# Performance work log

Measured on AMD Instinct MI355X. Metric: run time of the kernel, lower is better.

## Reference

```python
import jax, jax.numpy as jnp
import numpy as np

BS, H, S, DK = 4, 16, 1024, 64  # bs, n_heads, seq_len(=q_len), head_dim


def setup_inputs() -> dict:
    key = jax.random.key(0)
    k1, k2, k3, k4 = jax.random.split(key, 4)
    return {
        "q": jax.random.normal(k1, (BS, H, S, DK), dtype=jnp.float32),
        "k": jax.random.normal(k2, (BS, H, DK, S), dtype=jnp.float32),
        "v": jax.random.normal(k3, (BS, H, S, DK), dtype=jnp.float32),
        "prev": jax.random.normal(k4, (BS, H, S, S), dtype=jnp.float32),
        "attn_mask": jnp.zeros((1, S, S), dtype=jnp.float32),  # additive float mask
        "key_padding_mask": jnp.zeros((BS, S), dtype=bool),     # True = masked key
        "scale": jnp.asarray(DK ** -0.5, dtype=jnp.float32),    # learnable (lsa=True)
    }


def reference(q, k, v, prev, attn_mask, key_padding_mask, scale):
    # attn_scores = q @ k * scale + prev + attn_mask (float branch)
    scores = jnp.einsum("bhqd,bhdk->bhqk", q, k) * scale
    scores = scores + prev + attn_mask[:, None, :, :]  # [1,S,S] -> broadcast over b,h
    # key_padding_mask: [bs, seq_len] -> masked_fill(-inf)
    scores = jnp.where(key_padding_mask[:, None, None, :], -jnp.inf, scores)
    attn = jax.nn.softmax(scores, axis=-1)  # dropout p=0.0 -> identity
    out = jnp.einsum("bhqk,bhkd->bhqd", attn, v)
    # res_attention=True -> (output, attn_weights, attn_scores)
    return out, attn, scores
```

## Files before the change

### kernel.cpp

```cpp
#include <hip/hip_runtime.h>
#include <math.h>

#define SEQ 1024
#define DKH 64
#define QBLK 32
#define NTILE 16
#define ESTR 1028

typedef short s8v __attribute__((ext_vector_type(8)));
typedef short s4v __attribute__((ext_vector_type(4)));
typedef float f4v __attribute__((ext_vector_type(4)));

__device__ __forceinline__ short f2bf(float f) {
    unsigned u = __builtin_bit_cast(unsigned, f);
    return (short)((u + 0x8000u) >> 16);
}
__device__ __forceinline__ float bf2f(unsigned short h) {
    unsigned u = ((unsigned)h) << 16;
    return __builtin_bit_cast(float, u);
}
__device__ __forceinline__ s8v ld_frag(const unsigned short* p) {
    s4v a = *(const s4v*)(p);
    s4v b = *(const s4v*)(p + 4);
    s8v r;
    r[0]=a[0]; r[1]=a[1]; r[2]=a[2]; r[3]=a[3];
    r[4]=b[0]; r[5]=b[1]; r[6]=b[2]; r[7]=b[3];
    return r;
}

__global__ __launch_bounds__(512, 4)
void attn_fused(const float* __restrict__ q, const float* __restrict__ k,
                const float* __restrict__ v, const float* __restrict__ prev,
                const float* __restrict__ mask, const unsigned char* __restrict__ kpm,
                const float* __restrict__ scale_p,
                float* __restrict__ out, float* __restrict__ attn,
                float* __restrict__ scores)
{
    __shared__ unsigned short e_s[QBLK * ESTR];
    __shared__ float l_part[QBLK][4];
    __shared__ float inv_s[QBLK];

    const int t   = threadIdx.x;
    const int w   = t >> 6;
    const int rg  = w >> 2;
    const int cq  = w & 3;
    const int l   = t & 63;
    const int g   = l >> 4;
    const int c16 = l & 15;

    const int wg  = blockIdx.x;
    const int swz = (wg & 7) * 256 + (wg >> 3);
    const int bh  = swz >> 5;
    const int rt  = swz & 31;
    const int b   = bh >> 4;

    const float scale = *scale_p;

    const float* qb = q    + ((size_t)bh * SEQ + rt * QBLK) * DKH;
    const float* kb = k    + (size_t)bh * DKH * SEQ;
    const float* vb = v    + (size_t)bh * SEQ * DKH;
    const float* pb = prev + ((size_t)bh * SEQ + rt * QBLK) * SEQ;
    const float* mb = mask + (size_t)(rt * QBLK) * SEQ;
    const unsigned char* kp = kpm + (size_t)b * SEQ;
    float* sb = scores + ((size_t)bh * SEQ + rt * QBLK) * SEQ;
    float* ab = attn   + ((size_t)bh * SEQ + rt * QBLK) * SEQ;
    float* ob = out    + ((size_t)bh * SEQ + rt * QBLK) * DKH;

    {
        const int row = t >> 4, c0 = (t & 15) * 4;
        f4v f = *(const f4v*)(qb + row * DKH + c0);
        s4v h; h[0]=f2bf(f[0]); h[1]=f2bf(f[1]); h[2]=f2bf(f[2]); h[3]=f2bf(f[3]);
        *(s4v*)&e_s[row * ESTR + c0] = h;
    }
    __syncthreads();

    const s8v aq0 = ld_frag(&e_s[(rg * 16 + c16) * ESTR + g * 8]);
    const s8v aq1 = ld_frag(&e_s[(rg * 16 + c16) * ESTR + 32 + g * 8]);
    __syncthreads();

    const float* kcol = kb + (size_t)(g * 8) * SEQ + cq * 16 + c16;
    const float* vcol = vb + (size_t)(g * 8) * DKH + cq * 16 + c16;
    const float* prow0 = pb + (size_t)(rg * 16 + g * 4) * SEQ + cq * 16 + c16;
    const float* mrow0 = mb + (size_t)(rg * 16 + g * 4) * SEQ + cq * 16 + c16;

    float kraw[16], vraw[16];
    auto load_K = [&](int ct) {
        const float* p0 = kcol + ct * 64;
        #pragma unroll
        for (int ks = 0; ks < 2; ++ks)
            #pragma unroll
            for (int e = 0; e < 8; ++e)
                kraw[ks * 8 + e] = p0[(size_t)(ks * 32 + e) * SEQ];
    };
    auto load_V = [&](int ct) {
        const float* p0 = vcol + (size_t)(ct * 64) * DKH;
        #pragma unroll
        for (int cs = 0; cs < 2; ++cs)
            #pragma unroll
            for (int e = 0; e < 8; ++e)
                vraw[cs * 8 + e] = p0[(size_t)(cs * 32 + e) * DKH];
    };
    auto load_PM = [&](int ct, float (&pr)[4], float (&mr)[4], int& kf) {
        #pragma unroll
        for (int r = 0; r < 4; ++r) {
            pr[r] = __builtin_nontemporal_load(prow0 + (size_t)r * SEQ + ct * 64);
            mr[r] = mrow0[(size_t)r * SEQ + ct * 64];
        }
        kf = kp[ct * 64 + cq * 16 + c16];
    };

    float l_r[4] = {0.f, 0.f, 0.f, 0.f};
    f4v oacc = 0;

    float prA[4], mrA[4], prB[4], mrB[4];
    int kfA = 0, kfB = 0;
    load_K(0); load_V(0); load_PM(0, prA, mrA, kfA);

    auto tile = [&](int ct, float (&prc)[4], float (&mrc)[4], int kfc,
                    float (&prn)[4], float (&mrn)[4], int& kfn) {
        s8v ka, kb2;
        #pragma unroll
        for (int e = 0; e < 8; ++e) { ka[e] = f2bf(kraw[e]); kb2[e] = f2bf(kraw[8 + e]); }
        f4v acc = 0;
        acc = __builtin_amdgcn_mfma_f32_16x16x32_bf16(aq0, ka,  acc, 0, 0, 0);
        acc = __builtin_amdgcn_mfma_f32_16x16x32_bf16(aq1, kb2, acc, 0, 0, 0);
        if (ct + 1 < NTILE) load_K(ct + 1);

        const int colb = ct * 64 + cq * 16 + c16;
        #pragma unroll
        for (int r = 0; r < 4; ++r) {
            const int row = rg * 16 + g * 4 + r;
            float x = fmaf(acc[r], scale, prc[r] + mrc[r]);
            x = kfc ? -INFINITY : x;
            __builtin_nontemporal_store(x, sb + (size_t)row * SEQ + colb);
            const float e = __expf(x);
            l_r[r] += e;
            e_s[row * ESTR + colb] = (unsigned short)f2bf(e);
        }
        if (ct + 1 < NTILE) load_PM(ct + 1, prn, mrn, kfn);
        __syncthreads();

        const s8v ae0 = ld_frag(&e_s[(rg * 16 + c16) * ESTR + ct * 64 + g * 8]);
        const s8v ae1 = ld_frag(&e_s[(rg * 16 + c16) * ESTR + ct * 64 + 32 + g * 8]);
        s8v va, vb2;
        #pragma unroll
        for (int e = 0; e < 8; ++e) { va[e] = f2bf(vraw[e]); vb2[e] = f2bf(vraw[8 + e]); }
        oacc = __builtin_amdgcn_mfma_f32_16x16x32_bf16(ae0, va,  oacc, 0, 0, 0);
        oacc = __builtin_amdgcn_mfma_f32_16x16x32_bf16(ae1, vb2, oacc, 0, 0, 0);
        if (ct + 1 < NTILE) load_V(ct + 1);
    };

    for (int c2 = 0; c2 < NTILE; c2 += 2) {
        tile(c2,     prA, mrA, kfA, prB, mrB, kfB);
        tile(c2 + 1, prB, mrB, kfB, prA, mrA, kfA);
    }

    #pragma unroll
    for (int off = 1; off <= 8; off <<= 1) {
        #pragma unroll
        for (int r = 0; r < 4; ++r) l_r[r] += __shfl_xor(l_r[r], off, 64);
    }
    if (c16 == 0) {
        #pragma unroll
        for (int r = 0; r < 4; ++r) l_part[rg * 16 + g * 4 + r][cq] = l_r[r];
    }
    __syncthreads();
    if (t < QBLK)
        inv_s[t] = 1.0f / (l_part[t][0] + l_part[t][1] + l_part[t][2] + l_part[t][3]);
    __syncthreads();

    #pragma unroll
    for (int r = 0; r < 4; ++r) {
        const int row = rg * 16 + g * 4 + r;
        __builtin_nontemporal_store(oacc[r] * inv_s[row],
            ob + (size_t)row * DKH + cq * 16 + c16);
    }

    {
        const int row = t >> 4, i = t & 15;
        const float inv = inv_s[row];
        const unsigned short* erow = &e_s[row * ESTR];
        float* arow = ab + (size_t)row * SEQ;
        #pragma unroll
        for (int j = 0; j < 8; ++j) {
            const int c0 = (j * 16 + i) * 8;
            s8v h = ld_frag(erow + c0);
            f4v a0, a1;
            #pragma unroll
            for (int u = 0; u < 4; ++u) {
                a0[u] = bf2f((unsigned short)h[u]) * inv;
                a1[u] = bf2f((unsigned short)h[4 + u]) * inv;
            }
            __builtin_nontemporal_store(a0, (f4v*)(arow + c0));
            __builtin_nontemporal_store(a1, (f4v*)(arow + c0 + 4));
        }
    }
}

extern "C" void kernel_launch(void* const* d_in, const int* in_sizes, int n_in,
                              void* d_out, int out_size, void* d_ws, size_t ws_size,
                              hipStream_t stream) {
    const float* q    = (const float*)d_in[0];
    const float* k    = (const float*)d_in[1];
    const float* v    = (const float*)d_in[2];
    const float* prev = (const float*)d_in[3];
    const float* mask = (const float*)d_in[4];
    const unsigned char* kpm = (const unsigned char*)d_in[5];
    const float* scale = (const float*)d_in[6];

    float* out    = (float*)d_out;
    float* attn   = out  + (size_t)4 * 16 * SEQ * DKH;
    float* scores = attn + (size_t)4 * 16 * SEQ * SEQ;

    attn_fused<<<dim3(2048), dim3(512), 0, stream>>>(q, k, v, prev, mask, kpm, scale,
                                                     out, attn, scores);
}
```

Before: 326.5 us.

## Stage K/V through LDS with coalesced loads and halve the query block

K and V tiles are now read with coalesced float4 loads, converted to bf16 and transposed into shared-memory buffers. The MFMA B-fragments then come from LDS instead of from per-lane strided scalar gathers. The query block shrinks from 32 to 16 rows, so each block has 256 threads and the grid grows to 4096 blocks; the prev/mask double-buffering is dropped. This removes uncoalesced K/V global reads, at the cost of two extra barriers per tile and twice as many blocks each reading all of K/V.

```diff
diff --git a/kernel.cpp b/kernel.cpp
--- a/kernel.cpp
+++ b/kernel.cpp
@@ -3,9 +3,10 @@
 
 #define SEQ 1024
 #define DKH 64
-#define QBLK 32
+#define QBLK 16
 #define NTILE 16
-#define ESTR 1028
+#define KSTR 68
+#define ESTR 1032
 
 typedef short s8v __attribute__((ext_vector_type(8)));
 typedef short s4v __attribute__((ext_vector_type(4)));
@@ -28,7 +29,7 @@
     return r;
 }
 
-__global__ __launch_bounds__(512, 4)
+__global__ __launch_bounds__(256, 3)
 void attn_fused(const float* __restrict__ q, const float* __restrict__ k,
                 const float* __restrict__ v, const float* __restrict__ prev,
                 const float* __restrict__ mask, const unsigned char* __restrict__ kpm,
@@ -37,21 +38,22 @@
                 float* __restrict__ scores)
 {
     __shared__ unsigned short e_s[QBLK * ESTR];
+    __shared__ unsigned short k_s[64 * KSTR];
+    __shared__ unsigned short v_s[64 * KSTR];
     __shared__ float l_part[QBLK][4];
     __shared__ float inv_s[QBLK];
 
     const int t   = threadIdx.x;
     const int w   = t >> 6;
-    const int rg  = w >> 2;
-    const int cq  = w & 3;
     const int l   = t & 63;
     const int g   = l >> 4;
     const int c16 = l & 15;
+    const int sa  = t & 15, sg = t >> 4;
 
     const int wg  = blockIdx.x;
-    const int swz = (wg & 7) * 256 + (wg >> 3);
-    const int bh  = swz >> 5;
-    const int rt  = swz & 31;
+    const int swz = (wg & 7) * 512 + (wg >> 3);
+    const int bh  = swz >> 6;
+    const int rt  = swz & 63;
     const int b   = bh >> 4;
 
     const float scale = *scale_p;
@@ -73,86 +75,83 @@
         *(s4v*)&e_s[row * ESTR + c0] = h;
     }
     __syncthreads();
-
-    const s8v aq0 = ld_frag(&e_s[(rg * 16 + c16) * ESTR + g * 8]);
-    const s8v aq1 = ld_frag(&e_s[(rg * 16 + c16) * ESTR + 32 + g * 8]);
-    __syncthreads();
-
-    const float* kcol = kb + (size_t)(g * 8) * SEQ + cq * 16 + c16;
-    const float* vcol = vb + (size_t)(g * 8) * DKH + cq * 16 + c16;
-    const float* prow0 = pb + (size_t)(rg * 16 + g * 4) * SEQ + cq * 16 + c16;
-    const float* mrow0 = mb + (size_t)(rg * 16 + g * 4) * SEQ + cq * 16 + c16;
-
-    float kraw[16], vraw[16];
-    auto load_K = [&](int ct) {
-        const float* p0 = kcol + ct * 64;
-        #pragma unroll
-        for (int ks = 0; ks < 2; ++ks)
-            #pragma unroll
-            for (int e = 0; e < 8; ++e)
-                kraw[ks * 8 + e] = p0[(size_t)(ks * 32 + e) * SEQ];
+    const s8v aq0 = ld_frag(&e_s[c16 * ESTR + g * 8]);
+    const s8v aq1 = ld_frag(&e_s[c16 * ESTR + 32 + g * 8]);
+
+    f4v kreg[4], vreg[4];
+    auto load_KV = [&](int ct) {
+        const float* ksrc = kb + (size_t)(4 * sg) * SEQ + ct * 64 + 4 * sa;
+        kreg[0] = *(const f4v*)(ksrc);
+        kreg[1] = *(const f4v*)(ksrc + SEQ);
+        kreg[2] = *(const f4v*)(ksrc + 2 * SEQ);
+        kreg[3] = *(const f4v*)(ksrc + 3 * SEQ);
+        const float* vsrc = vb + (size_t)(ct * 64 + 4 * sg) * DKH + 4 * sa;
+        vreg[0] = *(const f4v*)(vsrc);
+        vreg[1] = *(const f4v*)(vsrc + DKH);
+        vreg[2] = *(const f4v*)(vsrc + 2 * DKH);
+        vreg[3] = *(const f4v*)(vsrc + 3 * DKH);
     };
-    auto load_V = [&](int ct) {
-        const float* p0 = vcol + (size_t)(ct * 64) * DKH;
-        #pragma unroll
-        for (int cs = 0; cs < 2; ++cs)
-            #pragma unroll
-            for (int e = 0; e < 8; ++e)
-                vraw[cs * 8 + e] = p0[(size_t)(cs * 32 + e) * DKH];
-    };
-    auto load_PM = [&](int ct, float (&pr)[4], float (&mr)[4], int& kf) {
+    float pr[4], mr[4];
+    int kf;
+    auto load_PM = [&](int ct) {
+        const int col = ct * 64 + w * 16 + c16;
         #pragma unroll
         for (int r = 0; r < 4; ++r) {
-            pr[r] = __builtin_nontemporal_load(prow0 + (size_t)r * SEQ + ct * 64);
-            mr[r] = mrow0[(size_t)r * SEQ + ct * 64];
-        }
-        kf = kp[ct * 64 + cq * 16 + c16];
+            pr[r] = __builtin_nontemporal_load(pb + (size_t)(g * 4 + r) * SEQ + col);
+            mr[r] = mb[(size_t)(g * 4 + r) * SEQ + col];
+        }
+        kf = kp[col];
     };
 
     float l_r[4] = {0.f, 0.f, 0.f, 0.f};
     f4v oacc = 0;
 
-    float prA[4], mrA[4], prB[4], mrB[4];
-    int kfA = 0, kfB = 0;
-    load_K(0); load_V(0); load_PM(0, prA, mrA, kfA);
-
-    auto tile = [&](int ct, float (&prc)[4], float (&mrc)[4], int kfc,
-                    float (&prn)[4], float (&mrn)[4], int& kfn) {
-        s8v ka, kb2;
-        #pragma unroll
-        for (int e = 0; e < 8; ++e) { ka[e] = f2bf(kraw[e]); kb2[e] = f2bf(kraw[8 + e]); }
+    load_KV(0);
+    load_PM(0);
+
+    for (int ct = 0; ct < NTILE; ++ct) {
+        __syncthreads();
+        #pragma unroll
+        for (int j = 0; j < 4; ++j) {
+            s4v hk; hk[0]=f2bf(kreg[0][j]); hk[1]=f2bf(kreg[1][j]); hk[2]=f2bf(kreg[2][j]); hk[3]=f2bf(kreg[3][j]);
+            *(s4v*)&k_s[(4 * sa + j) * KSTR + 4 * sg] = hk;
+            s4v hv; hv[0]=f2bf(vreg[0][j]); hv[1]=f2bf(vreg[1][j]); hv[2]=f2bf(vreg[2][j]); hv[3]=f2bf(vreg[3][j]);
+            *(s4v*)&v_s[(4 * sa + j) * KSTR + 4 * sg] = hv;
+        }
+        __syncthreads();
+
+        if (ct + 1 < NTILE) load_KV(ct + 1);
+
         f4v acc = 0;
-        acc = __builtin_amdgcn_mfma_f32_16x16x32_bf16(aq0, ka,  acc, 0, 0, 0);
-        acc = __builtin_amdgcn_mfma_f32_16x16x32_bf16(aq1, kb2, acc, 0, 0, 0);
-        if (ct + 1 < NTILE) load_K(ct + 1);
-
-        const int colb = ct * 64 + cq * 16 + c16;
+        {
+            const s8v bk0 = ld_frag(&k_s[(w * 16 + c16) * KSTR + g * 8]);
+            const s8v bk1 = ld_frag(&k_s[(w * 16 + c16) * KSTR + 32 + g * 8]);
+            acc = __builtin_amdgcn_mfma_f32_16x16x32_bf16(aq0, bk0, acc, 0, 0, 0);
+            acc = __builtin_amdgcn_mfma_f32_16x16x32_bf16(aq1, bk1, acc, 0, 0, 0);
+        }
+
+        const int colb = ct * 64 + w * 16 + c16;
         #pragma unroll
         for (int r = 0; r < 4; ++r) {
-            const int row = rg * 16 + g * 4 + r;
-            float x = fmaf(acc[r], scale, prc[r] + mrc[r]);
-            x = kfc ? -INFINITY : x;
+            const int row = g * 4 + r;
+            float x = fmaf(acc[r], scale, pr[r] + mr[r]);
+            x = kf ? -INFINITY : x;
             __builtin_nontemporal_store(x, sb + (size_t)row * SEQ + colb);
             const float e = __expf(x);
             l_r[r] += e;
             e_s[row * ESTR + colb] = (unsigned short)f2bf(e);
         }
-        if (ct + 1 < NTILE) load_PM(ct + 1, prn, mrn, kfn);
+        if (ct + 1 < NTILE) load_PM(ct + 1);
         __syncthreads();
 
-        const s8v ae0 = ld_frag(&e_s[(rg * 16 + c16) * ESTR + ct * 64 + g * 8]);
-        const s8v ae1 = ld_frag(&e_s[(rg * 16 + c16) * ESTR + ct * 64 + 32 + g * 8]);
-        s8v va, vb2;
-        #pragma unroll
-        for (int e = 0; e < 8; ++e) { va[e] = f2bf(vraw[e]); vb2[e] = f2bf(vraw[8 + e]); }
-        oacc = __builtin_amdgcn_mfma_f32_16x16x32_bf16(ae0, va,  oacc, 0, 0, 0);
-        oacc = __builtin_amdgcn_mfma_f32_16x16x32_bf16(ae1, vb2, oacc, 0, 0, 0);
-        if (ct + 1 < NTILE) load_V(ct + 1);
-    };
-
-    for (int c2 = 0; c2 < NTILE; c2 += 2) {
-        tile(c2,     prA, mrA, kfA, prB, mrB, kfB);
-        tile(c2 + 1, prB, mrB, kfB, prA, mrA, kfA);
+        {
+            const s8v ae0 = ld_frag(&e_s[c16 * ESTR + ct * 64 + g * 8]);
+            const s8v ae1 = ld_frag(&e_s[c16 * ESTR + ct * 64 + 32 + g * 8]);
+            const s8v bv0 = ld_frag(&v_s[(w * 16 + c16) * KSTR + g * 8]);
+            const s8v bv1 = ld_frag(&v_s[(w * 16 + c16) * KSTR + 32 + g * 8]);
+            oacc = __builtin_amdgcn_mfma_f32_16x16x32_bf16(ae0, bv0, oacc, 0, 0, 0);
+            oacc = __builtin_amdgcn_mfma_f32_16x16x32_bf16(ae1, bv1, oacc, 0, 0, 0);
+        }
     }
 
     #pragma unroll
@@ -162,7 +161,7 @@
     }
     if (c16 == 0) {
         #pragma unroll
-        for (int r = 0; r < 4; ++r) l_part[rg * 16 + g * 4 + r][cq] = l_r[r];
+        for (int r = 0; r < 4; ++r) l_part[g * 4 + r][w] = l_r[r];
     }
     __syncthreads();
     if (t < QBLK)
@@ -170,11 +169,9 @@
     __syncthreads();
 
     #pragma unroll
-    for (int r = 0; r < 4; ++r) {
-        const int row = rg * 16 + g * 4 + r;
-        __builtin_nontemporal_store(oacc[r] * inv_s[row],
-            ob + (size_t)row * DKH + cq * 16 + c16);
-    }
+    for (int r = 0; r < 4; ++r)
+        __builtin_nontemporal_store(oacc[r] * inv_s[g * 4 + r],
+            ob + (size_t)(g * 4 + r) * DKH + w * 16 + c16);
 
     {
         const int row = t >> 4, i = t & 15;
@@ -212,6 +209,6 @@
     float* attn   = out  + (size_t)4 * 16 * SEQ * DKH;
     float* scores = attn + (size_t)4 * 16 * SEQ * SEQ;
 
-    attn_fused<<<dim3(2048), dim3(512), 0, stream>>>(q, k, v, prev, mask, kpm, scale,
+    attn_fused<<<dim3(4096), dim3(256), 0, stream>>>(q, k, v, prev, mask, kpm, scale,
                                                      out, attn, scores);
 }
```

Result: faster. 306.7 us (-6.1%).
